# Performance work log

Measured on AMD Instinct MI355X. Metric: run time of the kernel, lower is better.

The kernel has to match this reference:

```python
import jax, jax.numpy as jnp
import numpy as np

NU, NT, NV = 20000, 50000, 100000   # user / travel / visit_area node counts
DU, DT = 64, 32                      # raw user / travel feature dims
H, L, E = 128, 8, 500000             # hidden, num_layers, edges per edge type
EPS = 1e-5


def _ln(x, g, b):
    m = x.mean(-1, keepdims=True)
    v = ((x - m) ** 2).mean(-1, keepdims=True)
    return (x - m) * jax.lax.rsqrt(v + EPS) * g + b


def _sage(x_src, x_dst, ei, Wl, bl, Wr, n_dst):
    # PyG SAGEConv: mean-aggregate source features over incoming edges,
    # transform with lin_l (bias), plus root transform lin_r (no bias).
    msg = jax.ops.segment_sum(x_src[ei[0]], ei[1], num_segments=n_dst)
    cnt = jax.ops.segment_sum(jnp.ones((ei.shape[1],), x_src.dtype), ei[1], num_segments=n_dst)
    mean = msg / jnp.maximum(cnt, 1.0)[:, None]
    return mean @ Wl + bl + x_dst @ Wr


def setup_inputs() -> dict:
    key = jax.random.key(0)
    ks = iter(jax.random.split(key, 64))
    f = lambda shape, s: jax.random.normal(next(ks), shape, jnp.float32) * s
    ei = lambda ns, nd: jnp.stack([
        jax.random.randint(next(ks), (E,), 0, ns, dtype=jnp.int32),
        jax.random.randint(next(ks), (E,), 0, nd, dtype=jnp.int32)])
    return {
        "x_user": jax.random.normal(next(ks), (NU, DU), jnp.float32),
        "x_travel": jax.random.normal(next(ks), (NT, DT), jnp.float32),
        "x_visit": jax.random.normal(next(ks), (NV, H), jnp.float32),
        "W_in_user": f((DU, H), 0.1), "b_in_user": jnp.zeros((H,), jnp.float32),
        "W_in_travel": f((DT, H), 0.1), "b_in_travel": jnp.zeros((H,), jnp.float32),
        # edge-type order: 0=user->travel, 1=travel->user, 2=travel->visit, 3=visit->travel
        "Wl": f((L, 4, H, H), 0.05), "bl": jnp.zeros((L, 4, H), jnp.float32),
        "Wr": f((L, 4, H, H), 0.05),
        # node-type order for norms: 0=user, 1=travel, 2=visit_area
        "ln_g": jnp.ones((L, 3, H), jnp.float32), "ln_b": jnp.zeros((L, 3, H), jnp.float32),
        # 3 expert MLPs (location / preference / category)
        "e_ln_g": jnp.ones((3, H), jnp.float32), "e_ln_b": jnp.zeros((3, H), jnp.float32),
        "e_W1": f((3, H, H), 0.05), "e_b1": jnp.zeros((3, H), jnp.float32),
        "e_W2": f((3, H, H // 2), 0.05), "e_b2": jnp.zeros((3, H // 2), jnp.float32),
        "e_W3": f((3, H // 2, 1), 0.05), "e_b3": jnp.zeros((3, 1), jnp.float32),
        # MultiheadAttention gate (4 heads) + learned query
        "attn_query": f((H,), 1.0),
        "Wq": f((H, H), 0.05), "bq": jnp.zeros((H,), jnp.float32),
        "Wk": f((H, H), 0.05), "bk": jnp.zeros((H,), jnp.float32),
        "Wv": f((H, H), 0.05), "bv": jnp.zeros((H,), jnp.float32),
        "Wo": f((H, H), 0.05), "bo": jnp.zeros((H,), jnp.float32),
        "f_ln_g": jnp.ones((H,), jnp.float32), "f_ln_b": jnp.zeros((H,), jnp.float32),
        "f_W1": f((H, H), 0.05), "f_b1": jnp.zeros((H,), jnp.float32),
        "f_W2": f((H, 1), 0.05), "f_b2": jnp.zeros((1,), jnp.float32),
        "ei_ut": ei(NU, NT), "ei_tu": ei(NT, NU),
        "ei_tv": ei(NT, NV), "ei_vt": ei(NV, NT),
    }


def reference(x_user, x_travel, x_visit,
              W_in_user, b_in_user, W_in_travel, b_in_travel,
              Wl, bl, Wr, ln_g, ln_b,
              e_ln_g, e_ln_b, e_W1, e_b1, e_W2, e_b2, e_W3, e_b3,
              attn_query, Wq, bq, Wk, bk, Wv, bv, Wo, bo,
              f_ln_g, f_ln_b, f_W1, f_b1, f_W2, f_b2,
              ei_ut, ei_tu, ei_tv, ei_vt):
    xu = x_user @ W_in_user + b_in_user
    xt = x_travel @ W_in_travel + b_in_travel
    xv = x_visit  # Identity projection
    for i in range(L):
        hu = _sage(xt, xu, ei_tu, Wl[i, 1], bl[i, 1], Wr[i, 1], NU)
        ht = (_sage(xu, xt, ei_ut, Wl[i, 0], bl[i, 0], Wr[i, 0], NT)
              + _sage(xv, xt, ei_vt, Wl[i, 3], bl[i, 3], Wr[i, 3], NT))  # HeteroConv aggr='sum'
        hv = _sage(xt, xv, ei_tv, Wl[i, 2], bl[i, 2], Wr[i, 2], NV)
        # dropout is identity in eval mode
        xu = jax.nn.relu(_ln(hu, ln_g[i, 0], ln_b[i, 0])) + xu
        xt = jax.nn.relu(_ln(ht, ln_g[i, 1], ln_b[i, 1])) + xt
        xv = jax.nn.relu(_ln(hv, ln_g[i, 2], ln_b[i, 2])) + xv
    h = xv  # [NV, H]
    # expert heads are computed in the torch forward but do NOT feed final_score
    _experts = [
        jax.nn.relu(jax.nn.relu(_ln(h, e_ln_g[j], e_ln_b[j]) @ e_W1[j] + e_b1[j])
                    @ e_W2[j] + e_b2[j]) @ e_W3[j] + e_b3[j]
        for j in range(3)
    ]
    # attention gate: 1 query token vs 1 key/value token per node -> softmax over 1 key == 1
    nh, hd = 4, H // 4
    Q = (attn_query @ Wq + bq).reshape(nh, hd)        # shared query
    Kh = (h @ Wk + bk).reshape(-1, nh, hd)
    Vh = (h @ Wv + bv).reshape(-1, nh, hd)
    s = (Q[None] * Kh).sum(-1) / jnp.sqrt(jnp.float32(hd))   # [NV, nh]
    w = jax.nn.softmax(s[..., None], axis=-1)                 # exactly ones
    attn = (w * Vh).reshape(-1, H) @ Wo + bo
    z = jax.nn.relu(_ln(attn, f_ln_g, f_ln_b) @ f_W1 + f_b1)  # final dropout = identity (eval)
    return (z @ f_W2 + f_b2)[:, 0]
```

## Files before the change

### kernel.cpp

```cpp
#include <hip/hip_runtime.h>

typedef float v4f __attribute__((ext_vector_type(4)));
typedef _Float16 h4 __attribute__((ext_vector_type(4)));
typedef _Float16 h8 __attribute__((ext_vector_type(8)));

namespace {

constexpr int NU = 20000;
constexpr int NT = 50000;
constexpr int NV = 100000;
constexpr int HD = 128;
constexpr int LAYERS = 8;
constexpr float EPS = 1e-5f;

constexpr int NUP = 20032, NTP = 50048, NVP = 100032;

constexpr int AGS = 136;
constexpr int HBS = 132;
constexpr int SCB = 2048;
constexpr int ECH = 2048;

constexpr int CAPT = 704;
constexpr int CAPUV = 1408;

__device__ __forceinline__ float wave_sum(float v) {
#pragma unroll
    for (int m = 32; m >= 1; m >>= 1) v += __shfl_xor(v, m, 64);
    return v;
}
__device__ __forceinline__ int wave_sum_i(int v) {
#pragma unroll
    for (int m = 32; m >= 1; m >>= 1) v += __shfl_xor(v, m, 64);
    return v;
}
__device__ __forceinline__ float qsum16(float v) {
#pragma unroll
    for (int m = 8; m >= 1; m >>= 1) v += __shfl_xor(v, m, 64);
    return v;
}


struct CsrJob {
    const int* src; const int* dst;
    int* cur; int* rp; int* col; float* inv;
    int n;
};
struct CsrJobs { CsrJob j[4]; };


__global__ __launch_bounds__(256) void hist_all_kernel(CsrJobs J, int E, int nbPer) {
    const int r = blockIdx.x & 7;
    const int rest = blockIdx.x >> 3;
    const int which = rest / nbPer;
    const int chunk = rest - which * nbPer;
    const CsrJob& job = J.j[which];
    const int n = job.n;
    const int lo = r * (n >> 3);
    const int hi = (r == 7) ? n : lo + (n >> 3);
    const int base = chunk * ECH;
    const int end = min(base + ECH, E);
    for (int e = base + threadIdx.x; e < end; e += 256) {
        const int d = job.dst[e];
        if (d >= lo && d < hi) atomicAdd(&job.cur[d], 1);
    }
}

__global__ __launch_bounds__(256) void csr_psum_kernel(CsrJobs J, int* __restrict__ part) {
    const int which = blockIdx.x >> 6;
    const int b = blockIdx.x & 63;
    const CsrJob& job = J.j[which];
    const int n = job.n;
    const int base = b * SCB;
    __shared__ int ws[4];
    int s = 0;
    if (base < n) {
        const int end = min(base + SCB, n);
        for (int i = base + threadIdx.x; i < end; i += 256) s += job.cur[i];
    }
    int sw = wave_sum_i(s);
    if ((threadIdx.x & 63) == 0) ws[threadIdx.x >> 6] = sw;
    __syncthreads();
    if (threadIdx.x == 0) part[which * 64 + b] = ws[0] + ws[1] + ws[2] + ws[3];
}

__global__ __launch_bounds__(64) void csr_pscan_kernel(int* __restrict__ part) {
    const int which = blockIdx.x;
    const int t = threadIdx.x;
    int v = part[which * 64 + t];
#pragma unroll
    for (int off = 1; off < 64; off <<= 1) {
        int u = __shfl_up(v, off, 64);
        if (t >= off) v += u;
    }
    int ex = __shfl_up(v, 1, 64);
    if (t == 0) ex = 0;
    part[which * 64 + t] = ex;
}

__global__ __launch_bounds__(256) void csr_scan_kernel(CsrJobs J, const int* __restrict__ part) {
    const int which = blockIdx.x >> 6;
    const int b = blockIdx.x & 63;
    const CsrJob& job = J.j[which];
    const int n = job.n;
    const int base = b * SCB;
    if (base >= n) return;
    const int t = threadIdx.x;
    __shared__ int tsum[256];
    int d[8];
    const int i0 = base + t * 8;
    int s = 0;
#pragma unroll
    for (int k = 0; k < 8; ++k) {
        const int i = i0 + k;
        d[k] = (i < n) ? job.cur[i] : 0;
        s += d[k];
    }
    tsum[t] = s;
    __syncthreads();
    for (int off = 1; off < 256; off <<= 1) {
        int u = (t >= off) ? tsum[t - off] : 0;
        __syncthreads();
        tsum[t] += u;
        __syncthreads();
    }
    int run = part[which * 64 + b] + ((t == 0) ? 0 : tsum[t - 1]);
#pragma unroll
    for (int k = 0; k < 8; ++k) {
        const int i = i0 + k;
        if (i < n) {
            job.rp[i] = run;
            job.inv[i] = 1.0f / (float)max(d[k], 1);
            job.cur[i] = run;
            run += d[k];
            if (i == n - 1) job.rp[n] = run;
        }
    }
}

__global__ __launch_bounds__(256) void scatter_all_kernel(CsrJobs J, int E, int nbPer) {
    const int r = blockIdx.x & 7;
    const int rest = blockIdx.x >> 3;
    const int which = rest / nbPer;
    const int chunk = rest - which * nbPer;
    const CsrJob& job = J.j[which];
    const int n = job.n;
    const int lo = r * (n >> 3);
    const int hi = (r == 7) ? n : lo + (n >> 3);
    const int base = chunk * ECH;
    const int end = min(base + ECH, E);
    for (int e = base + threadIdx.x; e < end; e += 256) {
        const int d = job.dst[e];
        if (d >= lo && d < hi) {
            int p = atomicAdd(&job.cur[d], 1);
            job.col[p] = job.src[e];
        }
    }
}


__global__ __launch_bounds__(256) void tw_kernel(const float* __restrict__ Wl,
                                                 const float* __restrict__ Wr,
                                                 _Float16* __restrict__ WT) {
    const int slot = blockIdx.x;
    const int layer = slot / 7, j = slot % 7;
    const float* A;
    const float* B = nullptr;
    if (j < 4) A = Wl + ((size_t)layer * 4 + j) * 16384;
    else if (j == 4) {
        A = Wr + ((size_t)layer * 4 + 0) * 16384;
        B = Wr + ((size_t)layer * 4 + 3) * 16384;
    } else A = Wr + ((size_t)layer * 4 + (j - 4)) * 16384;
    _Float16* o = WT + (size_t)slot * 16384;
    for (int idx = threadIdx.x; idx < 16384; idx += 256) {
        const int n = idx >> 7, k = idx & 127;
        float v = A[k * 128 + n];
        if (j == 4) v += B[k * 128 + n];
        o[idx] = (_Float16)v;
    }
}


__global__ __launch_bounds__(256) void cast_kernel(const float* __restrict__ X,
                                                   _Float16* __restrict__ Y, int n4) {
    int i = blockIdx.x * 256 + threadIdx.x;
    if (i < n4) {
        v4f x = *(const v4f*)(X + (size_t)i * 4);
        h4 y;
        y[0] = (_Float16)x.x; y[1] = (_Float16)x.y;
        y[2] = (_Float16)x.z; y[3] = (_Float16)x.w;
        *(h4*)(Y + (size_t)i * 4) = y;
    }
}


#define ACC_H8(vh, X, Y)                                                         \
    {                                                                            \
        X.x += (float)vh[0]; X.y += (float)vh[1];                                \
        X.z += (float)vh[2]; X.w += (float)vh[3];                                \
        Y.x += (float)vh[4]; Y.y += (float)vh[5];                                \
        Y.z += (float)vh[6]; Y.w += (float)vh[7];                                \
    }

__device__ __forceinline__ void gather_row_h(
    const _Float16* __restrict__ src, const int* __restrict__ colg,
    const int* __restrict__ sCol, int off_r, int s0, int e1,
    int c8, float iv, _Float16* __restrict__ outRow, int cap) {
    const int d = e1 - s0;
    const int jst = min(d, max(0, cap - off_r));
    v4f aA = {0.f, 0.f, 0.f, 0.f}, aB = aA, bA = aA, bB = aA;
    int j = 0;
    for (; j + 8 <= jst; j += 8) {
        h8 v0 = *(const h8*)(src + (size_t)sCol[off_r + j + 0] * 128 + c8);
        h8 v1 = *(const h8*)(src + (size_t)sCol[off_r + j + 1] * 128 + c8);
        h8 v2 = *(const h8*)(src + (size_t)sCol[off_r + j + 2] * 128 + c8);
        h8 v3 = *(const h8*)(src + (size_t)sCol[off_r + j + 3] * 128 + c8);
        h8 v4 = *(const h8*)(src + (size_t)sCol[off_r + j + 4] * 128 + c8);
        h8 v5 = *(const h8*)(src + (size_t)sCol[off_r + j + 5] * 128 + c8);
        h8 v6 = *(const h8*)(src + (size_t)sCol[off_r + j + 6] * 128 + c8);
        h8 v7 = *(const h8*)(src + (size_t)sCol[off_r + j + 7] * 128 + c8);
        ACC_H8(v0, aA, aB); ACC_H8(v1, bA, bB);
        ACC_H8(v2, aA, aB); ACC_H8(v3, bA, bB);
        ACC_H8(v4, aA, aB); ACC_H8(v5, bA, bB);
        ACC_H8(v6, aA, aB); ACC_H8(v7, bA, bB);
    }
    for (; j < jst; ++j) {
        h8 v0 = *(const h8*)(src + (size_t)sCol[off_r + j] * 128 + c8);
        ACC_H8(v0, aA, aB);
    }
    for (int e = s0 + jst; e < e1; ++e) {
        h8 v0 = *(const h8*)(src + (size_t)colg[e] * 128 + c8);
        ACC_H8(v0, aA, aB);
    }
    v4f r0 = (aA + bA) * iv;
    v4f r1 = (aB + bB) * iv;
    h8 o;
    o[0] = (_Float16)r0.x; o[1] = (_Float16)r0.y; o[2] = (_Float16)r0.z; o[3] = (_Float16)r0.w;
    o[4] = (_Float16)r1.x; o[5] = (_Float16)r1.y; o[6] = (_Float16)r1.z; o[7] = (_Float16)r1.w;
    *(h8*)(outRow + c8) = o;
}


template <int HAS2>
__device__ __forceinline__ void sage_mfma_body(
    int row0, int nrows,
    const float* __restrict__ xdst, float* __restrict__ out,
    _Float16* __restrict__ out_h, const _Float16* __restrict__ xdh,
    const _Float16* __restrict__ src1h, const int* __restrict__ rp1,
    const int* __restrict__ col1, const float* __restrict__ inv1,
    const _Float16* __restrict__ Wl1T, const float* __restrict__ bl1,
    const _Float16* __restrict__ src2h, const int* __restrict__ rp2,
    const int* __restrict__ col2, const float* __restrict__ inv2,
    const _Float16* __restrict__ Wl2T, const float* __restrict__ bl2,
    const _Float16* __restrict__ WrTh,
    const float* __restrict__ g, const float* __restrict__ bln,
    _Float16* aggH1, _Float16* aggH2, float* hbuf, int* sC1, int* sC2, int cap) {
    const int t = threadIdx.x;
    const int w = t >> 6, l = t & 63;
    const int m = l & 15, q = l >> 4;
    const int c8 = m * 8;
    const int rows_end = min(row0 + 64, nrows);

    const int eb1 = rp1[row0];
    const int cnt1 = min(rp1[rows_end] - eb1, cap);
    for (int i = t; i < cnt1; i += 256) sC1[i] = col1[eb1 + i];
    int eb2 = 0;
    if constexpr (HAS2) {
        eb2 = rp2[row0];
        const int cnt2 = min(rp2[rows_end] - eb2, cap);
        for (int i = t; i < cnt2; i += 256) sC2[i] = col2[eb2 + i];
    }
    __syncthreads();

#pragma unroll
    for (int i = 0; i < 4; ++i) {
        const int rloc = w * 16 + q * 4 + i;
        const int gr = row0 + rloc;
        if (gr < nrows) {
            {
                const int s0 = rp1[gr], e1r = rp1[gr + 1];
                gather_row_h(src1h, col1, sC1, s0 - eb1, s0, e1r, c8, inv1[gr],
                             aggH1 + (size_t)rloc * AGS, cap);
            }
            if constexpr (HAS2) {
                const int s0 = rp2[gr], e1r = rp2[gr + 1];
                gather_row_h(src2h, col2, sC2, s0 - eb2, s0, e1r, c8, inv2[gr],
                             aggH2 + (size_t)rloc * AGS, cap);
            }
        }
    }

    v4f acc[8];
#pragma unroll
    for (int nt = 0; nt < 8; ++nt) acc[nt] = (v4f){0.f, 0.f, 0.f, 0.f};

    const _Float16* xdrow = xdh + (size_t)(row0 + w * 16 + m) * 128;
#pragma unroll
    for (int kt = 0; kt < 4; ++kt) {
        h8 a = *(const h8*)(xdrow + kt * 32 + q * 8);
#pragma unroll
        for (int nt = 0; nt < 8; ++nt) {
            h8 b = *(const h8*)(WrTh + (size_t)(nt * 16 + m) * 128 + kt * 32 + q * 8);
            acc[nt] = __builtin_amdgcn_mfma_f32_16x16x32_f16(a, b, acc[nt], 0, 0, 0);
        }
    }
    __syncthreads();

    const _Float16* arow1 = aggH1 + (size_t)(w * 16 + m) * AGS;
#pragma unroll
    for (int kt = 0; kt < 4; ++kt) {
        h8 a = *(const h8*)(arow1 + kt * 32 + q * 8);
#pragma unroll
        for (int nt = 0; nt < 8; ++nt) {
            h8 b = *(const h8*)(Wl1T + (size_t)(nt * 16 + m) * 128 + kt * 32 + q * 8);
            acc[nt] = __builtin_amdgcn_mfma_f32_16x16x32_f16(a, b, acc[nt], 0, 0, 0);
        }
    }
    if constexpr (HAS2) {
        const _Float16* arow2 = aggH2 + (size_t)(w * 16 + m) * AGS;
#pragma unroll
        for (int kt = 0; kt < 4; ++kt) {
            h8 a = *(const h8*)(arow2 + kt * 32 + q * 8);
#pragma unroll
            for (int nt = 0; nt < 8; ++nt) {
                h8 b = *(const h8*)(Wl2T + (size_t)(nt * 16 + m) * 128 + kt * 32 + q * 8);
                acc[nt] = __builtin_amdgcn_mfma_f32_16x16x32_f16(a, b, acc[nt], 0, 0, 0);
            }
        }
    }
    __syncthreads();

#pragma unroll
    for (int nt = 0; nt < 8; ++nt)
#pragma unroll
        for (int r = 0; r < 4; ++r)
            hbuf[(size_t)(w * 16 + q * 4 + r) * HBS + nt * 16 + m] = acc[nt][r];
    __syncthreads();

    v4f bg0 = *(const v4f*)&bl1[c8];
    v4f bg1 = *(const v4f*)&bl1[c8 + 4];
    if constexpr (HAS2) {
        bg0 += *(const v4f*)&bl2[c8];
        bg1 += *(const v4f*)&bl2[c8 + 4];
    }
    v4f g0 = *(const v4f*)&g[c8], g1 = *(const v4f*)&g[c8 + 4];
    v4f lb0 = *(const v4f*)&bln[c8], lb1 = *(const v4f*)&bln[c8 + 4];
#pragma unroll
    for (int i = 0; i < 4; ++i) {
        const int rloc = w * 16 + q * 4 + i;
        const int gr = row0 + rloc;
        if (gr >= nrows) continue;
        v4f h0 = *(const v4f*)&hbuf[(size_t)rloc * HBS + c8] + bg0;
        v4f h1 = *(const v4f*)&hbuf[(size_t)rloc * HBS + c8 + 4] + bg1;
        float part = h0.x + h0.y + h0.z + h0.w + h1.x + h1.y + h1.z + h1.w;
        float mean = qsum16(part) * (1.0f / 128.0f);
        v4f d0 = h0 - mean, d1 = h1 - mean;
        float vp = d0.x * d0.x + d0.y * d0.y + d0.z * d0.z + d0.w * d0.w +
                   d1.x * d1.x + d1.y * d1.y + d1.z * d1.z + d1.w * d1.w;
        float var = qsum16(vp) * (1.0f / 128.0f);
        float rs = rsqrtf(var + EPS);
        v4f x0 = *(const v4f*)&xdst[(size_t)gr * 128 + c8];
        v4f x1 = *(const v4f*)&xdst[(size_t)gr * 128 + c8 + 4];
        v4f y0, y1;
#pragma unroll
        for (int e = 0; e < 4; ++e) {
            y0[e] = fmaxf(d0[e] * rs * g0[e] + lb0[e], 0.f) + x0[e];
            y1[e] = fmaxf(d1[e] * rs * g1[e] + lb1[e], 0.f) + x1[e];
        }
        *(v4f*)&out[(size_t)gr * 128 + c8] = y0;
        *(v4f*)&out[(size_t)gr * 128 + c8 + 4] = y1;
        h8 oh;
#pragma unroll
        for (int e = 0; e < 4; ++e) {
            oh[e] = (_Float16)y0[e];
            oh[4 + e] = (_Float16)y1[e];
        }
        *(h8*)&out_h[(size_t)gr * 128 + c8] = oh;
    }
}

struct TrvParams {
    const float* xdst; float* out; _Float16* out_h; const _Float16* xdh;
    const _Float16* src1h; const int* rp1; const int* col1; const float* inv1;
    const _Float16* Wl1T; const float* bl1;
    const _Float16* src2h; const int* rp2; const int* col2; const float* inv2;
    const _Float16* Wl2T; const float* bl2;
    const _Float16* WrTh; const float* g; const float* bln;
};

struct UpdParams {
    const float* xdst; float* out; _Float16* out_h; const _Float16* xdh;
    const _Float16* srch; const int* rp; const int* col; const float* inv;
    const _Float16* WlT; const float* bl; const _Float16* WrT;
    const float* g; const float* bln;
    int nrows;
};

__global__ __launch_bounds__(256, 4) void layer_mfma(TrvParams T, UpdParams U, UpdParams V,
                                                     int nbT, int nbU) {
    __shared__ __align__(16) char smem[34816 + 5632];
    int b = blockIdx.x;
    if (b < nbT) {
        _Float16* aggH1 = (_Float16*)smem;
        _Float16* aggH2 = (_Float16*)(smem + 17408);
        float* hbuf = (float*)smem;
        int* sC1 = (int*)(smem + 34816);
        int* sC2 = sC1 + CAPT;
        sage_mfma_body<1>(b * 64, NT, T.xdst, T.out, T.out_h, T.xdh,
                          T.src1h, T.rp1, T.col1, T.inv1, T.Wl1T, T.bl1,
                          T.src2h, T.rp2, T.col2, T.inv2, T.Wl2T, T.bl2,
                          T.WrTh, T.g, T.bln, aggH1, aggH2, hbuf, sC1, sC2, CAPT);
    } else {
        b -= nbT;
        const bool isU = b < nbU;
        const UpdParams& P = isU ? U : V;
        const int row0 = (isU ? b : b - nbU) * 64;
        _Float16* aggH1 = (_Float16*)smem;
        float* hbuf = (float*)smem;
        int* sC1 = (int*)(smem + 34816);
        sage_mfma_body<0>(row0, P.nrows, P.xdst, P.out, P.out_h, P.xdh,
                          P.srch, P.rp, P.col, P.inv, P.WlT, P.bl,
                          nullptr, nullptr, nullptr, nullptr, nullptr, nullptr,
                          P.WrT, P.g, P.bln, aggH1, nullptr, hbuf, sC1, nullptr, CAPUV);
    }
}


template <int K, bool LN_IN, bool RELU, bool MIRROR>
__global__ __launch_bounds__(256) void gemm_kernel(const float* __restrict__ X,
                                                   const float* __restrict__ W,
                                                   const float* __restrict__ bias,
                                                   float* __restrict__ Y,
                                                   _Float16* __restrict__ Yh,
                                                   const float* __restrict__ g,
                                                   const float* __restrict__ bln) {
    static_assert(!LN_IN || K == 128, "LN input requires K==128");
    __shared__ __align__(16) float As[16 * K];
    const int t = threadIdx.x;
    const size_t row0 = (size_t)blockIdx.x * 16;

    for (int idx = t; idx < 16 * K; idx += 256) As[idx] = X[row0 * K + idx];
    __syncthreads();

    if (LN_IN) {
        const int w = t >> 6, l = t & 63;
        for (int qq = 0; qq < 4; ++qq) {
            const int r = w * 4 + qq;
            float a0 = As[r * K + l], a1 = As[r * K + 64 + l];
            float mm = wave_sum(a0 + a1) * (1.0f / 128.0f);
            float d0 = a0 - mm, d1 = a1 - mm;
            float var = wave_sum(d0 * d0 + d1 * d1) * (1.0f / 128.0f);
            float rs = rsqrtf(var + EPS);
            As[r * K + l] = d0 * rs * g[l] + bln[l];
            As[r * K + 64 + l] = d1 * rs * g[64 + l] + bln[64 + l];
        }
        __syncthreads();
    }

    const int c0 = (t & 31) * 4;
    const int r0 = (t >> 5) * 2;
    v4f b4 = *(const v4f*)&bias[c0];
    v4f acc0 = b4, acc1 = b4;
#pragma unroll 4
    for (int k = 0; k < K; k += 4) {
        v4f a0 = *(const v4f*)&As[r0 * K + k];
        v4f a1 = *(const v4f*)&As[(r0 + 1) * K + k];
        v4f w0 = *(const v4f*)&W[(size_t)(k + 0) * HD + c0];
        v4f w1 = *(const v4f*)&W[(size_t)(k + 1) * HD + c0];
        v4f w2 = *(const v4f*)&W[(size_t)(k + 2) * HD + c0];
        v4f w3 = *(const v4f*)&W[(size_t)(k + 3) * HD + c0];
        acc0 += a0.x * w0 + a0.y * w1 + a0.z * w2 + a0.w * w3;
        acc1 += a1.x * w0 + a1.y * w1 + a1.z * w2 + a1.w * w3;
    }
    if (RELU) {
#pragma unroll
        for (int i = 0; i < 4; ++i) {
            acc0[i] = fmaxf(acc0[i], 0.0f);
            acc1[i] = fmaxf(acc1[i], 0.0f);
        }
    }
    *(v4f*)&Y[(row0 + r0) * HD + c0] = acc0;
    *(v4f*)&Y[(row0 + r0 + 1) * HD + c0] = acc1;
    if (MIRROR) {
        h4 m0, m1;
#pragma unroll
        for (int i = 0; i < 4; ++i) {
            m0[i] = (_Float16)acc0[i];
            m1[i] = (_Float16)acc1[i];
        }
        *(h4*)&Yh[(row0 + r0) * HD + c0] = m0;
        *(h4*)&Yh[(row0 + r0 + 1) * HD + c0] = m1;
    }
}


__global__ __launch_bounds__(128) void fold_kernel(const float* __restrict__ Wv,
                                                   const float* __restrict__ bv,
                                                   const float* __restrict__ Wo,
                                                   const float* __restrict__ bo,
                                                   float* __restrict__ Wvo,
                                                   float* __restrict__ bvo) {
    const int c = threadIdx.x;
    const int r = blockIdx.x;
    if (r < 128) {
        float s = 0.f;
        for (int k = 0; k < 128; ++k) s += Wv[r * 128 + k] * Wo[k * 128 + c];
        Wvo[r * 128 + c] = s;
    } else {
        float s = bo[c];
        for (int k = 0; k < 128; ++k) s += bv[k] * Wo[k * 128 + c];
        bvo[c] = s;
    }
}


__global__ __launch_bounds__(256) void dot_kernel(const float* __restrict__ Z,
                                                  const float* __restrict__ w2,
                                                  const float* __restrict__ b2,
                                                  float* __restrict__ out, int n) {
    const int w = threadIdx.x >> 6, l = threadIdx.x & 63;
    const size_t row = (size_t)blockIdx.x * 4 + w;
    if (row < (size_t)n) {
        float v = Z[row * 128 + l] * w2[l] + Z[row * 128 + 64 + l] * w2[64 + l];
        v = wave_sum(v);
        if (l == 0) out[row] = v + b2[0];
    }
}

}

extern "C" void kernel_launch(void* const* d_in, const int* in_sizes, int n_in,
                              void* d_out, int out_size, void* d_ws, size_t ws_size,
                              hipStream_t stream) {
    const float* x_user     = (const float*)d_in[0];
    const float* x_travel   = (const float*)d_in[1];
    float*       xv         = (float*)d_in[2];
    const float* W_in_user  = (const float*)d_in[3];
    const float* b_in_user  = (const float*)d_in[4];
    const float* W_in_travel= (const float*)d_in[5];
    const float* b_in_travel= (const float*)d_in[6];
    const float* Wl         = (const float*)d_in[7];
    const float* bl         = (const float*)d_in[8];
    const float* Wr         = (const float*)d_in[9];
    const float* ln_g       = (const float*)d_in[10];
    const float* ln_b       = (const float*)d_in[11];
    const float* Wv_        = (const float*)d_in[25];
    const float* bv_        = (const float*)d_in[26];
    const float* Wo_        = (const float*)d_in[27];
    const float* bo_        = (const float*)d_in[28];
    const float* f_ln_g     = (const float*)d_in[29];
    const float* f_ln_b     = (const float*)d_in[30];
    const float* f_W1       = (const float*)d_in[31];
    const float* f_b1       = (const float*)d_in[32];
    const float* f_W2       = (const float*)d_in[33];
    const float* f_b2       = (const float*)d_in[34];
    const int*   ei_ut      = (const int*)d_in[35];
    const int*   ei_tu      = (const int*)d_in[36];
    const int*   ei_tv      = (const int*)d_in[37];
    const int*   ei_vt      = (const int*)d_in[38];
    const int E = in_sizes[35] / 2;

    constexpr size_t FUSED_NEED = (size_t)140 << 20;
    const bool fused = ws_size >= FUSED_NEED;

    char* wsb = (char*)d_ws;
    size_t off = 0;
    auto alloc = [&](size_t bytes) -> void* {
        off = (off + 511) & ~(size_t)511;
        void* p = wsb + off;
        off += bytes;
        return p;
    };
    float* xu = (float*)alloc((size_t)NU * HD * 4);
    float* xt = (float*)alloc((size_t)NT * HD * 4);
    _Float16* xu_h[2];
    _Float16* xv_h[2];
    _Float16* xt_h[2];
    xu_h[0] = (_Float16*)alloc((size_t)NUP * HD * 2);
    xv_h[0] = (_Float16*)alloc((size_t)NVP * HD * 2);
    xt_h[0] = (_Float16*)alloc((size_t)NTP * HD * 2);
    xt_h[1] = (_Float16*)alloc((size_t)NTP * HD * 2);
    if (fused) {
        xu_h[1] = (_Float16*)alloc((size_t)NUP * HD * 2);
        xv_h[1] = (_Float16*)alloc((size_t)NVP * HD * 2);
    } else {
        xu_h[1] = xu_h[0];
        xv_h[1] = xv_h[0];
    }
    _Float16* WT = (_Float16*)alloc((size_t)LAYERS * 7 * 16384 * 2);
    float* Wvo = (float*)alloc(128 * 128 * 4);
    float* bvo = (float*)alloc(128 * 4);
    int* part = (int*)alloc(4 * 64 * 4);

    const int ndst[4] = {NU, NT, NT, NV};
    int* cur4 = (int*)alloc((size_t)(NU + NT + NT + NV) * 4);
    int *rp[4], *colb[4];
    float* invb[4];
    int* cur[4];
    {
        int coff = 0;
        for (int i = 0; i < 4; ++i) {
            cur[i] = cur4 + coff;
            coff += ndst[i];
            rp[i]   = (int*)alloc((size_t)(ndst[i] + 1) * 4);
            colb[i] = (int*)alloc((size_t)E * 4);
            invb[i] = (float*)alloc((size_t)ndst[i] * 4);
        }
    }

    hipMemsetAsync(cur4, 0, (size_t)(NU + NT + NT + NV) * 4, stream);
    CsrJobs J;
    J.j[0] = { ei_tu, ei_tu + E, cur[0], rp[0], colb[0], invb[0], NU };
    J.j[1] = { ei_ut, ei_ut + E, cur[1], rp[1], colb[1], invb[1], NT };
    J.j[2] = { ei_vt, ei_vt + E, cur[2], rp[2], colb[2], invb[2], NT };
    J.j[3] = { ei_tv, ei_tv + E, cur[3], rp[3], colb[3], invb[3], NV };
    const int nbPerC = (E + ECH - 1) / ECH;
    hist_all_kernel<<<4 * nbPerC * 8, 256, 0, stream>>>(J, E, nbPerC);
    csr_psum_kernel<<<4 * 64, 256, 0, stream>>>(J, part);
    csr_pscan_kernel<<<4, 64, 0, stream>>>(part);
    csr_scan_kernel<<<4 * 64, 256, 0, stream>>>(J, part);
    scatter_all_kernel<<<4 * nbPerC * 8, 256, 0, stream>>>(J, E, nbPerC);

    tw_kernel<<<LAYERS * 7, 256, 0, stream>>>(Wl, Wr, WT);

    gemm_kernel<64, false, false, true><<<NU / 16, 256, 0, stream>>>(
        x_user, W_in_user, b_in_user, xu, xu_h[0], nullptr, nullptr);
    gemm_kernel<32, false, false, true><<<NT / 16, 256, 0, stream>>>(
        x_travel, W_in_travel, b_in_travel, xt, xt_h[0], nullptr, nullptr);
    cast_kernel<<<(NV * HD / 4 + 255) / 256, 256, 0, stream>>>(xv, xv_h[0], NV * HD / 4);

    const int nbU = (NU + 63) / 64;
    const int nbV = (NV + 63) / 64;
    const int nbT = (NT + 63) / 64;
    for (int i = 0; i < LAYERS; ++i) {
        const _Float16* WTl = WT + (size_t)i * 7 * 16384;
        const float* bl_i = bl + (size_t)i * 4 * 128;
        const float* g_i  = ln_g + (size_t)i * 3 * 128;
        const float* b_i  = ln_b + (size_t)i * 3 * 128;
        const int c = i & 1, nx = c ^ 1;
        TrvParams T = { xt, xt, xt_h[nx], xt_h[c],
                        xu_h[c], rp[1], colb[1], invb[1], WTl + 0 * 16384, bl_i + 0 * 128,
                        xv_h[c], rp[2], colb[2], invb[2], WTl + 3 * 16384, bl_i + 3 * 128,
                        WTl + 4 * 16384, g_i + 1 * 128, b_i + 1 * 128 };
        UpdParams U = { xu, xu, xu_h[nx], xu_h[c], xt_h[c], rp[0], colb[0], invb[0],
                        WTl + 1 * 16384, bl_i + 1 * 128, WTl + 5 * 16384,
                        g_i + 0 * 128, b_i + 0 * 128, NU };
        UpdParams V = { xv, xv, xv_h[nx], xv_h[c], xt_h[c], rp[3], colb[3], invb[3],
                        WTl + 2 * 16384, bl_i + 2 * 128, WTl + 6 * 16384,
                        g_i + 2 * 128, b_i + 2 * 128, NV };
        if (fused) {
            layer_mfma<<<nbT + nbU + nbV, 256, 0, stream>>>(T, U, V, nbT, nbU);
        } else {
            layer_mfma<<<nbT, 256, 0, stream>>>(T, U, V, nbT, nbU);
            layer_mfma<<<nbU + nbV, 256, 0, stream>>>(T, U, V, 0, nbU);
        }
    }

    fold_kernel<<<129, 128, 0, stream>>>(Wv_, bv_, Wo_, bo_, Wvo, bvo);
    float* attn = (float*)xu_h[0];
    gemm_kernel<128, false, false, false><<<NV / 16, 256, 0, stream>>>(
        xv, Wvo, bvo, attn, nullptr, nullptr, nullptr);
    gemm_kernel<128, true, true, false><<<NV / 16, 256, 0, stream>>>(
        attn, f_W1, f_b1, attn, nullptr, f_ln_g, f_ln_b);
    dot_kernel<<<NV / 4, 256, 0, stream>>>(attn, f_W2, f_b2, (float*)d_out, NV);
}
```

Baseline: 2.249 ms.

## Shrink layer LDS footprint by reusing one aggregation buffer and in-register LayerNorm

The travel path now gathers the second edge type into the same LDS aggregation buffer after the first MFMA pass, instead of using two buffers. The LayerNorm epilogue reads the MFMA accumulators directly from registers and drops the fp32 staging buffer in LDS, which halves shared memory per block and lets the launch bound request 7 waves per SIMD. The overflow gather loop is also unrolled by 8 to expose more memory parallelism. In exchange it adds barriers, serialises the two gathers with the MFMA work, and writes the epilogue output with strided scalar stores instead of vector stores.

```diff
diff --git a/kernel.cpp b/kernel.cpp
--- a/kernel.cpp
+++ b/kernel.cpp
@@ -16,7 +16,6 @@
 constexpr int NUP = 20032, NTP = 50048, NVP = 100032;
 
 constexpr int AGS = 136;
-constexpr int HBS = 132;
 constexpr int SCB = 2048;
 constexpr int ECH = 2048;
 
@@ -227,7 +226,24 @@
         h8 v0 = *(const h8*)(src + (size_t)sCol[off_r + j] * 128 + c8);
         ACC_H8(v0, aA, aB);
     }
-    for (int e = s0 + jst; e < e1; ++e) {
+    int e = s0 + jst;
+    for (; e + 8 <= e1; e += 8) {
+        const int cc0 = colg[e + 0], cc1 = colg[e + 1], cc2 = colg[e + 2], cc3 = colg[e + 3];
+        const int cc4 = colg[e + 4], cc5 = colg[e + 5], cc6 = colg[e + 6], cc7 = colg[e + 7];
+        h8 v0 = *(const h8*)(src + (size_t)cc0 * 128 + c8);
+        h8 v1 = *(const h8*)(src + (size_t)cc1 * 128 + c8);
+        h8 v2 = *(const h8*)(src + (size_t)cc2 * 128 + c8);
+        h8 v3 = *(const h8*)(src + (size_t)cc3 * 128 + c8);
+        h8 v4 = *(const h8*)(src + (size_t)cc4 * 128 + c8);
+        h8 v5 = *(const h8*)(src + (size_t)cc5 * 128 + c8);
+        h8 v6 = *(const h8*)(src + (size_t)cc6 * 128 + c8);
+        h8 v7 = *(const h8*)(src + (size_t)cc7 * 128 + c8);
+        ACC_H8(v0, aA, aB); ACC_H8(v1, bA, bB);
+        ACC_H8(v2, aA, aB); ACC_H8(v3, bA, bB);
+        ACC_H8(v4, aA, aB); ACC_H8(v5, bA, bB);
+        ACC_H8(v6, aA, aB); ACC_H8(v7, bA, bB);
+    }
+    for (; e < e1; ++e) {
         h8 v0 = *(const h8*)(src + (size_t)colg[e] * 128 + c8);
         ACC_H8(v0, aA, aB);
     }
@@ -253,7 +269,7 @@
     const _Float16* __restrict__ Wl2T, const float* __restrict__ bl2,
     const _Float16* __restrict__ WrTh,
     const float* __restrict__ g, const float* __restrict__ bln,
-    _Float16* aggH1, _Float16* aggH2, float* hbuf, int* sC1, int* sC2, int cap) {
+    _Float16* aggH, int* sC1, int* sC2, int cap) {
     const int t = threadIdx.x;
     const int w = t >> 6, l = t & 63;
     const int m = l & 15, q = l >> 4;
@@ -276,16 +292,9 @@
         const int rloc = w * 16 + q * 4 + i;
         const int gr = row0 + rloc;
         if (gr < nrows) {
-            {
-                const int s0 = rp1[gr], e1r = rp1[gr + 1];
-                gather_row_h(src1h, col1, sC1, s0 - eb1, s0, e1r, c8, inv1[gr],
-                             aggH1 + (size_t)rloc * AGS, cap);
-            }
-            if constexpr (HAS2) {
-                const int s0 = rp2[gr], e1r = rp2[gr + 1];
-                gather_row_h(src2h, col2, sC2, s0 - eb2, s0, e1r, c8, inv2[gr],
-                             aggH2 + (size_t)rloc * AGS, cap);
-            }
+            const int s0 = rp1[gr], e1r = rp1[gr + 1];
+            gather_row_h(src1h, col1, sC1, s0 - eb1, s0, e1r, c8, inv1[gr],
+                         aggH + (size_t)rloc * AGS, cap);
         }
     }
 
@@ -305,10 +314,10 @@
     }
     __syncthreads();
 
-    const _Float16* arow1 = aggH1 + (size_t)(w * 16 + m) * AGS;
+    const _Float16* arow = aggH + (size_t)(w * 16 + m) * AGS;
 #pragma unroll
     for (int kt = 0; kt < 4; ++kt) {
-        h8 a = *(const h8*)(arow1 + kt * 32 + q * 8);
+        h8 a = *(const h8*)(arow + kt * 32 + q * 8);
 #pragma unroll
         for (int nt = 0; nt < 8; ++nt) {
             h8 b = *(const h8*)(Wl1T + (size_t)(nt * 16 + m) * 128 + kt * 32 + q * 8);
@@ -316,10 +325,21 @@
         }
     }
     if constexpr (HAS2) {
-        const _Float16* arow2 = aggH2 + (size_t)(w * 16 + m) * AGS;
+        __syncthreads();
+#pragma unroll
+        for (int i = 0; i < 4; ++i) {
+            const int rloc = w * 16 + q * 4 + i;
+            const int gr = row0 + rloc;
+            if (gr < nrows) {
+                const int s0 = rp2[gr], e1r = rp2[gr + 1];
+                gather_row_h(src2h, col2, sC2, s0 - eb2, s0, e1r, c8, inv2[gr],
+                             aggH + (size_t)rloc * AGS, cap);
+            }
+        }
+        __syncthreads();
 #pragma unroll
         for (int kt = 0; kt < 4; ++kt) {
-            h8 a = *(const h8*)(arow2 + kt * 32 + q * 8);
+            h8 a = *(const h8*)(arow + kt * 32 + q * 8);
 #pragma unroll
             for (int nt = 0; nt < 8; ++nt) {
                 h8 b = *(const h8*)(Wl2T + (size_t)(nt * 16 + m) * 128 + kt * 32 + q * 8);
@@ -327,54 +347,42 @@
             }
         }
     }
-    __syncthreads();
-
-#pragma unroll
-    for (int nt = 0; nt < 8; ++nt)
-#pragma unroll
-        for (int r = 0; r < 4; ++r)
-            hbuf[(size_t)(w * 16 + q * 4 + r) * HBS + nt * 16 + m] = acc[nt][r];
-    __syncthreads();
-
-    v4f bg0 = *(const v4f*)&bl1[c8];
-    v4f bg1 = *(const v4f*)&bl1[c8 + 4];
-    if constexpr (HAS2) {
-        bg0 += *(const v4f*)&bl2[c8];
-        bg1 += *(const v4f*)&bl2[c8 + 4];
-    }
-    v4f g0 = *(const v4f*)&g[c8], g1 = *(const v4f*)&g[c8 + 4];
-    v4f lb0 = *(const v4f*)&bln[c8], lb1 = *(const v4f*)&bln[c8 + 4];
-#pragma unroll
-    for (int i = 0; i < 4; ++i) {
-        const int rloc = w * 16 + q * 4 + i;
-        const int gr = row0 + rloc;
+
+    float bgv[8];
+#pragma unroll
+    for (int nt = 0; nt < 8; ++nt) {
+        bgv[nt] = bl1[nt * 16 + m];
+        if constexpr (HAS2) bgv[nt] += bl2[nt * 16 + m];
+    }
+#pragma unroll
+    for (int r = 0; r < 4; ++r) {
+        const int gr = row0 + w * 16 + q * 4 + r;
         if (gr >= nrows) continue;
-        v4f h0 = *(const v4f*)&hbuf[(size_t)rloc * HBS + c8] + bg0;
-        v4f h1 = *(const v4f*)&hbuf[(size_t)rloc * HBS + c8 + 4] + bg1;
-        float part = h0.x + h0.y + h0.z + h0.w + h1.x + h1.y + h1.z + h1.w;
-        float mean = qsum16(part) * (1.0f / 128.0f);
-        v4f d0 = h0 - mean, d1 = h1 - mean;
-        float vp = d0.x * d0.x + d0.y * d0.y + d0.z * d0.z + d0.w * d0.w +
-                   d1.x * d1.x + d1.y * d1.y + d1.z * d1.z + d1.w * d1.w;
-        float var = qsum16(vp) * (1.0f / 128.0f);
-        float rs = rsqrtf(var + EPS);
-        v4f x0 = *(const v4f*)&xdst[(size_t)gr * 128 + c8];
-        v4f x1 = *(const v4f*)&xdst[(size_t)gr * 128 + c8 + 4];
-        v4f y0, y1;
-#pragma unroll
-        for (int e = 0; e < 4; ++e) {
-            y0[e] = fmaxf(d0[e] * rs * g0[e] + lb0[e], 0.f) + x0[e];
-            y1[e] = fmaxf(d1[e] * rs * g1[e] + lb1[e], 0.f) + x1[e];
-        }
-        *(v4f*)&out[(size_t)gr * 128 + c8] = y0;
-        *(v4f*)&out[(size_t)gr * 128 + c8 + 4] = y1;
-        h8 oh;
-#pragma unroll
-        for (int e = 0; e < 4; ++e) {
-            oh[e] = (_Float16)y0[e];
-            oh[4 + e] = (_Float16)y1[e];
-        }
-        *(h8*)&out_h[(size_t)gr * 128 + c8] = oh;
+        float h[8];
+        float part = 0.f;
+#pragma unroll
+        for (int nt = 0; nt < 8; ++nt) {
+            h[nt] = acc[nt][r] + bgv[nt];
+            part += h[nt];
+        }
+        const float mean = qsum16(part) * (1.0f / 128.0f);
+        float vp = 0.f;
+#pragma unroll
+        for (int nt = 0; nt < 8; ++nt) {
+            h[nt] -= mean;
+            vp += h[nt] * h[nt];
+        }
+        const float rs = rsqrtf(qsum16(vp) * (1.0f / 128.0f) + EPS);
+        const float* xr = xdst + (size_t)gr * 128;
+        float* orow = out + (size_t)gr * 128;
+        _Float16* ohrow = out_h + (size_t)gr * 128;
+#pragma unroll
+        for (int nt = 0; nt < 8; ++nt) {
+            const int cc = nt * 16 + m;
+            const float y = fmaxf(h[nt] * rs * g[cc] + bln[cc], 0.f) + xr[cc];
+            orow[cc] = y;
+            ohrow[cc] = (_Float16)y;
+        }
     }
 }
 
@@ -395,32 +403,27 @@
     int nrows;
 };
 
-__global__ __launch_bounds__(256, 4) void layer_mfma(TrvParams T, UpdParams U, UpdParams V,
+__global__ __launch_bounds__(256, 7) void layer_mfma(TrvParams T, UpdParams U, UpdParams V,
                                                      int nbT, int nbU) {
-    __shared__ __align__(16) char smem[34816 + 5632];
+    __shared__ __align__(16) char smem[17408 + 5632];
+    _Float16* aggH = (_Float16*)smem;
+    int* sC1 = (int*)(smem + 17408);
     int b = blockIdx.x;
     if (b < nbT) {
-        _Float16* aggH1 = (_Float16*)smem;
-        _Float16* aggH2 = (_Float16*)(smem + 17408);
-        float* hbuf = (float*)smem;
-        int* sC1 = (int*)(smem + 34816);
         int* sC2 = sC1 + CAPT;
         sage_mfma_body<1>(b * 64, NT, T.xdst, T.out, T.out_h, T.xdh,
                           T.src1h, T.rp1, T.col1, T.inv1, T.Wl1T, T.bl1,
                           T.src2h, T.rp2, T.col2, T.inv2, T.Wl2T, T.bl2,
-                          T.WrTh, T.g, T.bln, aggH1, aggH2, hbuf, sC1, sC2, CAPT);
+                          T.WrTh, T.g, T.bln, aggH, sC1, sC2, CAPT);
     } else {
         b -= nbT;
         const bool isU = b < nbU;
         const UpdParams& P = isU ? U : V;
         const int row0 = (isU ? b : b - nbU) * 64;
-        _Float16* aggH1 = (_Float16*)smem;
-        float* hbuf = (float*)smem;
-        int* sC1 = (int*)(smem + 34816);
         sage_mfma_body<0>(row0, P.nrows, P.xdst, P.out, P.out_h, P.xdh,
                           P.srch, P.rp, P.col, P.inv, P.WlT, P.bl,
                           nullptr, nullptr, nullptr, nullptr, nullptr, nullptr,
-                          P.WrT, P.g, P.bln, aggH1, nullptr, hbuf, sC1, nullptr, CAPUV);
+                          P.WrT, P.g, P.bln, aggH, sC1, nullptr, CAPUV);
     }
 }
 
```

Measured after the change: 2.345 ms. +4.2%, slower.
